# Optimization experiments

Hardware: AMD Instinct MI355X
Metric: run time of the kernel (lower is better)

## Reference

```python
import jax, jax.numpy as jnp
import numpy as np

N = 100000   # nodes
E = 1600000  # edges
F = 64       # num_features
H = 64       # hidden_units
C = 10       # num_classes
G = 1000     # graphs in batch
BN_EPS = 1e-5


def setup_inputs() -> dict:
    key = jax.random.key(0)
    ks = jax.random.split(key, 32)
    inp = {
        "x": jax.random.normal(ks[0], (N, F), dtype=jnp.float32),
        "edge_index": jax.random.randint(ks[1], (2, E), 0, N, dtype=jnp.int64),
        "batch": jnp.sort(jax.random.randint(ks[2], (N,), 0, G, dtype=jnp.int64)),
    }
    i = 3
    def w(shape, scale):
        nonlocal i
        a = jax.random.normal(ks[i], shape, dtype=jnp.float32) * scale
        i += 1
        return a
    for l, din in [(0, F), (1, H)]:
        inp[f"c{l}_w1"] = w((din, H), 1.0 / np.sqrt(din))
        inp[f"c{l}_b1"] = jnp.zeros((H,), jnp.float32)
        inp[f"c{l}_g1"] = jnp.ones((H,), jnp.float32)
        inp[f"c{l}_be1"] = jnp.zeros((H,), jnp.float32)
        inp[f"c{l}_w2"] = w((H, H), 1.0 / np.sqrt(H))
        inp[f"c{l}_b2"] = jnp.zeros((H,), jnp.float32)
        inp[f"bn{l}_g"] = jnp.ones((H,), jnp.float32)
        inp[f"bn{l}_b"] = jnp.zeros((H,), jnp.float32)
    for l, din in [(0, F), (1, H), (2, H)]:
        inp[f"l{l}_w"] = w((din, C), 1.0 / np.sqrt(din))
        inp[f"l{l}_b"] = jnp.zeros((C,), jnp.float32)
    return inp


def _bn(h, g, b):
    # BatchNorm1d in training mode: batch statistics over node axis
    m = jnp.mean(h, axis=0)
    v = jnp.var(h, axis=0)
    return g * (h - m) * jax.lax.rsqrt(v + BN_EPS) + b


def _gin_conv(h, src, dst, w1, b1, g1, be1, w2, b2):
    # scatter-add neighbor aggregation: out[dst] += h[src]; eps = 0
    agg = jax.ops.segment_sum(h[src], dst, num_segments=N)
    z = h + agg                      # (1 + eps) * x + sum_j x_j
    z = jax.nn.relu(_bn(z @ w1 + b1, g1, be1))
    return z @ w2 + b2


def reference(x, edge_index, batch,
              c0_w1, c0_b1, c0_g1, c0_be1, c0_w2, c0_b2, bn0_g, bn0_b,
              c1_w1, c1_b1, c1_g1, c1_be1, c1_w2, c1_b2, bn1_g, bn1_b,
              l0_w, l0_b, l1_w, l1_b, l2_w, l2_b):
    src, dst = edge_index[0], edge_index[1]
    h0 = x
    h1 = jax.nn.relu(_bn(_gin_conv(h0, src, dst, c0_w1, c0_b1, c0_g1, c0_be1, c0_w2, c0_b2), bn0_g, bn0_b))
    h2 = jax.nn.relu(_bn(_gin_conv(h1, src, dst, c1_w1, c1_b1, c1_g1, c1_be1, c1_w2, c1_b2), bn1_g, bn1_b))
    # jumping-knowledge readout: per-layer global_add_pool -> Linear -> sum (dropout=0)
    out = jnp.zeros((G, C), dtype=x.dtype)
    for h, w, b in [(h0, l0_w, l0_b), (h1, l1_w, l1_b), (h2, l2_w, l2_b)]:
        pooled = jax.ops.segment_sum(h, batch, num_segments=G)
        out = out + pooled @ w + b
    return out
```

## Files before the change

kernel.cpp:

```cpp
#include <hip/hip_runtime.h>
#include <hip/hip_bf16.h>

#define BN_EPS 1e-5f
#define NBMAX 512
#define CHUNK 4096
#define CAP   5120
#define PCAP  7168

typedef __hip_bfloat16 bf16;
typedef __attribute__((ext_vector_type(8))) short short8;
typedef __attribute__((ext_vector_type(4))) float f32x4;

__device__ __forceinline__ float b2f(bf16 v) { return __bfloat162float(v); }
__device__ __forceinline__ bf16 f2b(float v) { return __float2bfloat16(v); }
__device__ __forceinline__ float bl(unsigned u) { return __uint_as_float(u << 16); }
__device__ __forceinline__ float bh(unsigned u) { return __uint_as_float(u & 0xffff0000u); }
__device__ __forceinline__ unsigned pack2(float x, float y) {
    union { bf16 b[2]; unsigned u; } p;
    p.b[0] = f2b(x); p.b[1] = f2b(y);
    return p.u;
}
__device__ __forceinline__ float bs2f(short s) {
    return __uint_as_float(((unsigned)(unsigned short)s) << 16);
}
__device__ __forceinline__ short f2bs(float v) {
    bf16 b = f2b(v);
    return *reinterpret_cast<short*>(&b);
}

__global__ __launch_bounds__(256) void initcast_k(
    const float* __restrict__ in, bf16* __restrict__ out, int n4, int total4,
    int* __restrict__ bcur, int NB)
{
    if (blockIdx.x == 0) {
        for (int i = threadIdx.x; i < NB; i += 256) bcur[i] = i * CAP;
    }
    int i = blockIdx.x * 256 + threadIdx.x;
    if (i >= total4) return;
    if (i < n4) {
        float4 v = ((const float4*)in)[i];
        union { ushort4 u; bf16 b[4]; } p;
        p.b[0] = f2b(v.x); p.b[1] = f2b(v.y); p.b[2] = f2b(v.z); p.b[3] = f2b(v.w);
        ((ushort4*)out)[i] = p.u;
    } else {
        ushort4 z; z.x = 0; z.y = 0; z.z = 0; z.w = 0;
        ((ushort4*)out)[i] = z;
    }
}

__global__ __launch_bounds__(256) void binscatter_k(
    const int* __restrict__ src, const int* __restrict__ dst,
    int* __restrict__ bcur, int* __restrict__ tmp, int E, int NB)
{
    __shared__ int hist[NBMAX];
    __shared__ int loff[NBMAX];
    __shared__ int gb[NBMAX];
    __shared__ int lcur[NBMAX];
    __shared__ int staged[CHUNK];
    __shared__ unsigned short sb[CHUNK];
    __shared__ int ssc[256];
    const int t = threadIdx.x;
    for (int i = t; i < NB; i += 256) { hist[i] = 0; lcur[i] = 0; }
    __syncthreads();
    const int base = blockIdx.x * CHUNK;
    const int lim = min(CHUNK, E - base);
    int myb[16], myw[16];
    int cnt = 0;
    for (int i = t; i < lim; i += 256) {
        int d = dst[base + i];
        int s_ = src[base + i];
        int b = d >> 8;
        myb[cnt] = b;
        myw[cnt] = (s_ << 8) | (d & 255);
        cnt++;
        atomicAdd(&hist[b], 1);
    }
    __syncthreads();
    int v0 = (2 * t     < NB) ? hist[2 * t]     : 0;
    int v1 = (2 * t + 1 < NB) ? hist[2 * t + 1] : 0;
    ssc[t] = v0 + v1;
    __syncthreads();
    for (int off = 1; off < 256; off <<= 1) {
        int a = (t >= off) ? ssc[t - off] : 0;
        __syncthreads();
        ssc[t] += a;
        __syncthreads();
    }
    int excl = ssc[t] - (v0 + v1);
    if (2 * t < NB)     loff[2 * t] = excl;
    if (2 * t + 1 < NB) loff[2 * t + 1] = excl + v0;
    __syncthreads();
    for (int b = t; b < NB; b += 256)
        if (hist[b] > 0) gb[b] = atomicAdd(&bcur[b], hist[b]);
    for (int i = 0; i < cnt; i++) {
        int b = myb[i];
        int p = loff[b] + atomicAdd(&lcur[b], 1);
        staged[p] = myw[i];
        sb[p] = (unsigned short)b;
    }
    __syncthreads();
    for (int i = t; i < lim; i += 256) {
        int b = sb[i];
        tmp[gb[b] + (i - loff[b])] = staged[i];
    }
}

__global__ __launch_bounds__(256) void csr_k(
    const int* __restrict__ bcur, const int* __restrict__ tmp,
    int* __restrict__ rowptr, int* __restrict__ rowend,
    int* __restrict__ adj, int N)
{
    __shared__ int hist[256], pfx[256], cur[256], ssc[256];
    __shared__ int sadj[PCAP];
    const int b = blockIdx.x, t = threadIdx.x;
    const int lo = b * CAP;
    const int plo = b * PCAP;
    const int cnt = min(bcur[b] - lo, CAP);
    hist[t] = 0; cur[t] = 0;
    __syncthreads();
    for (int i = t; i < cnt; i += 256)
        atomicAdd(&hist[tmp[lo + i] & 255], 1);
    __syncthreads();
    const int v = hist[t];
    const int pv = (v + 7) & ~7;
    ssc[t] = pv;
    __syncthreads();
    for (int off = 1; off < 256; off <<= 1) {
        int a = (t >= off) ? ssc[t - off] : 0;
        __syncthreads();
        ssc[t] += a;
        __syncthreads();
    }
    const int myp = ssc[t] - pv;
    pfx[t] = myp;
    const int node = b * 256 + t;
    if (node < N) {
        rowptr[node] = plo + myp;
        rowend[node] = plo + myp + pv;
    }
    __syncthreads();
    const int pcnt = ssc[255];
    for (int i = t; i < cnt; i += 256) {
        int w = tmp[lo + i];
        int d = w & 255;
        int p = pfx[d] + atomicAdd(&cur[d], 1);
        sadj[p] = w >> 8;
    }
    __syncthreads();
    for (int i = v; i < pv; i++) sadj[myp + i] = N;
    __syncthreads();
    for (int i = t; i < pcnt; i += 256) adj[plo + i] = sadj[i];
}

__global__ __launch_bounds__(256, 4) void aggregate_k(
    const bf16* __restrict__ h, const int* __restrict__ rowptr,
    const int* __restrict__ rowend, const int* __restrict__ adj,
    bf16* __restrict__ z, int N)
{
    const int lane16 = threadIdx.x & 15;
    const int n = blockIdx.x * 16 + (threadIdx.x >> 4);
    if (n >= N) return;
    const char* hb_ = (const char*)h;
    const int b = rowptr[n], e = rowend[n];

    uint2 u = *(const uint2*)(hb_ + ((size_t)n << 7) + (lane16 << 3));
    float s0 = bl(u.x), s1 = bh(u.x), s2 = bl(u.y), s3 = bh(u.y);

    int m[8];
    if (b < e) {
        #pragma unroll
        for (int k = 0; k < 8; k++) m[k] = adj[b + k];
    }
    for (int i = b; i < e; ) {
        uint2 w[8];
        #pragma unroll
        for (int k = 0; k < 8; k++)
            w[k] = *(const uint2*)(hb_ + (((size_t)(unsigned)m[k]) << 7) + (lane16 << 3));
        const int inext = i + 8;
        if (inext < e) {
            #pragma unroll
            for (int k = 0; k < 8; k++) m[k] = adj[inext + k];
        }
        #pragma unroll
        for (int k = 0; k < 8; k++) {
            s0 += bl(w[k].x); s1 += bh(w[k].x);
            s2 += bl(w[k].y); s3 += bh(w[k].y);
        }
        i = inext;
    }
    uint2 o;
    o.x = pack2(s0, s1);
    o.y = pack2(s2, s3);
    *(uint2*)((char*)z + ((size_t)n << 7) + (lane16 << 3)) = o;
}

__global__ __launch_bounds__(256) void ewact_k(
    const bf16* __restrict__ y, const float* __restrict__ sc,
    const float* __restrict__ sh, bf16* __restrict__ h, int N)
{
    const int idx = blockIdx.x * 256 + threadIdx.x;
    const int total = (N + 1) * 8;
    if (idx >= total) return;
    short8 v;
    if (idx < N * 8) {
        const int f0 = (idx & 7) * 8;
        v = *(const short8*)(y + (size_t)idx * 8);
        #pragma unroll
        for (int j = 0; j < 8; j++)
            v[j] = f2bs(fmaxf(fmaf(bs2f(v[j]), sc[f0 + j], sh[f0 + j]), 0.f));
    } else {
        #pragma unroll
        for (int j = 0; j < 8; j++) v[j] = 0;
    }
    *(short8*)(h + (size_t)idx * 8) = v;
}

template<int MODE>
__global__ __launch_bounds__(256) void gemm64_k(
    const bf16* __restrict__ A,
    const float* __restrict__ scin, const float* __restrict__ shin,
    const float* __restrict__ W, const float* __restrict__ bias,
    bf16* __restrict__ out, float* __restrict__ pstat, int nrows)
{
    __shared__ bf16 sWt[64][72];
    __shared__ bf16 sC[128][68];
    __shared__ float sSc[64], sSh[64], sB[64];
    __shared__ float sredS[64][17], sredQ[64][17];
    const int tid = threadIdx.x;

    if (tid < 64) {
        sB[tid] = bias[tid];
        if (MODE == 1) { sSc[tid] = scin[tid]; sSh[tid] = shin[tid]; }
    }
    for (int i = tid; i < 4096; i += 256) {
        int k = i >> 6, n = i & 63;
        sWt[n][k] = f2b(W[i]);
    }
    __syncthreads();

    const int wave = tid >> 6, lane = tid & 63;
    const int quad = lane >> 4, l16 = lane & 15;
    const int row0 = blockIdx.x * 128 + wave * 32;

    short8 a[2][2];
    #pragma unroll
    for (int rt = 0; rt < 2; rt++) {
        int r = row0 + rt * 16 + l16;
        int rr = min(r, nrows - 1);
        const bf16* arow = A + (size_t)rr * 64;
        a[rt][0] = *(const short8*)(arow + quad * 8);
        a[rt][1] = *(const short8*)(arow + 32 + quad * 8);
        if (MODE == 1) {
            #pragma unroll
            for (int j = 0; j < 8; j++) {
                int f0 = quad * 8 + j;
                a[rt][0][j] = f2bs(fmaxf(fmaf(bs2f(a[rt][0][j]), sSc[f0], sSh[f0]), 0.f));
                int f1 = 32 + f0;
                a[rt][1][j] = f2bs(fmaxf(fmaf(bs2f(a[rt][1][j]), sSc[f1], sSh[f1]), 0.f));
            }
        }
    }

    float psS[4], psQ[4];
    #pragma unroll
    for (int t = 0; t < 4; t++) { psS[t] = 0.f; psQ[t] = 0.f; }

    #pragma unroll
    for (int t = 0; t < 4; t++) {
        const int n = t * 16 + l16;
        short8 b0 = *(const short8*)&sWt[n][quad * 8];
        short8 b1 = *(const short8*)&sWt[n][32 + quad * 8];
        const float bn_ = sB[n];
        #pragma unroll
        for (int rt = 0; rt < 2; rt++) {
            f32x4 acc = {0.f, 0.f, 0.f, 0.f};
            acc = __builtin_amdgcn_mfma_f32_16x16x32_bf16(a[rt][0], b0, acc, 0, 0, 0);
            acc = __builtin_amdgcn_mfma_f32_16x16x32_bf16(a[rt][1], b1, acc, 0, 0, 0);
            #pragma unroll
            for (int reg = 0; reg < 4; reg++) {
                const int lr = wave * 32 + rt * 16 + quad * 4 + reg;
                float v = acc[reg] + bn_;
                sC[lr][n] = f2b(v);
                if (row0 + rt * 16 + quad * 4 + reg < nrows) {
                    psS[t] += v;
                    psQ[t] = fmaf(v, v, psQ[t]);
                }
            }
        }
    }

    #pragma unroll
    for (int t = 0; t < 4; t++) {
        sredS[t * 16 + l16][wave * 4 + quad] = psS[t];
        sredQ[t * 16 + l16][wave * 4 + quad] = psQ[t];
    }
    __syncthreads();

    const int gbase = blockIdx.x * 128;
    #pragma unroll
    for (int it = 0; it < 8; it++) {
        int idx = it * 256 + tid;
        int r = idx >> 4, c4 = idx & 15;
        if (gbase + r < nrows) {
            ushort4 v = *(const ushort4*)&sC[r][c4 * 4];
            *(ushort4*)(out + (size_t)(gbase + r) * 64 + c4 * 4) = v;
        }
    }

    if (tid < 128) {
        const int c = tid & 63;
        const float* p = (tid < 64) ? &sredS[c][0] : &sredQ[c][0];
        float s = 0.f;
        #pragma unroll
        for (int i = 0; i < 16; i++) s += p[i];
        pstat[(size_t)blockIdx.x * 128 + (tid < 64 ? c : 64 + c)] = s;
    }
}

__global__ __launch_bounds__(256) void bn_reduce_k(
    const float* __restrict__ pstat, int nblk,
    const float* __restrict__ g, const float* __restrict__ be, float invN,
    float* __restrict__ sc, float* __restrict__ sh)
{
    const int f = blockIdx.x;
    const int t = threadIdx.x;
    float S = 0.f, Q = 0.f;
    for (int b = t; b < nblk; b += 256) {
        S += pstat[(size_t)b * 128 + f];
        Q += pstat[(size_t)b * 128 + 64 + f];
    }
    __shared__ float rs[256], rq[256];
    rs[t] = S; rq[t] = Q;
    __syncthreads();
    for (int off = 128; off > 0; off >>= 1) {
        if (t < off) { rs[t] += rs[t + off]; rq[t] += rq[t + off]; }
        __syncthreads();
    }
    if (t == 0) {
        float m = rs[0] * invN;
        float v = rq[0] * invN - m * m;
        float s = g[f] * rsqrtf(v + BN_EPS);
        sc[f] = s;
        sh[f] = be[f] - m * s;
    }
}

__global__ __launch_bounds__(256) void pool_readout_k(
    const bf16* __restrict__ xb, const bf16* __restrict__ h1,
    const bf16* __restrict__ y1, const int* __restrict__ batch,
    const float* __restrict__ scB, const float* __restrict__ shB,
    const float* __restrict__ w0, const float* __restrict__ b0,
    const float* __restrict__ w1, const float* __restrict__ b1,
    const float* __restrict__ w2, const float* __restrict__ b2,
    float* __restrict__ out, int Nn)
{
    const int g = blockIdx.x;
    int lo = 0, hi = Nn;
    while (lo < hi) { int mid = (lo + hi) >> 1; if (batch[mid] < g) lo = mid + 1; else hi = mid; }
    const int start = lo;
    hi = Nn;
    while (lo < hi) { int mid = (lo + hi) >> 1; if (batch[mid] <= g) lo = mid + 1; else hi = mid; }
    const int end = lo;

    const int f = threadIdx.x & 63;
    const int w = threadIdx.x >> 6;
    const float sB = scB[f], tB = shB[f];

    float s0 = 0.f, s1 = 0.f, s2 = 0.f;
    for (int i = start + w; i < end; i += 4) {
        s0 += b2f(xb[(size_t)i * 64 + f]);
        s1 += b2f(h1[(size_t)i * 64 + f]);
        s2 += fmaxf(fmaf(b2f(y1[(size_t)i * 64 + f]), sB, tB), 0.f);
    }
    __shared__ float p[3][4][64];
    p[0][w][f] = s0; p[1][w][f] = s1; p[2][w][f] = s2;
    __syncthreads();
    if (threadIdx.x < 10) {
        const int c = threadIdx.x;
        float acc = b0[c] + b1[c] + b2[c];
        for (int k = 0; k < 64; k++) {
            float q0 = p[0][0][k] + p[0][1][k] + p[0][2][k] + p[0][3][k];
            float q1 = p[1][0][k] + p[1][1][k] + p[1][2][k] + p[1][3][k];
            float q2 = p[2][0][k] + p[2][1][k] + p[2][2][k] + p[2][3][k];
            acc = fmaf(q0, w0[k * 10 + c], acc);
            acc = fmaf(q1, w1[k * 10 + c], acc);
            acc = fmaf(q2, w2[k * 10 + c], acc);
        }
        out[(size_t)g * 10 + c] = acc;
    }
}

extern "C" void kernel_launch(void* const* d_in, const int* in_sizes, int n_in,
                              void* d_out, int out_size, void* d_ws, size_t ws_size,
                              hipStream_t stream)
{
    const float* x     = (const float*)d_in[0];
    const int*   edge  = (const int*)d_in[1];
    const int*   batch = (const int*)d_in[2];
    const int N = in_sizes[0] / 64;
    const int E = in_sizes[1] / 2;
    const int G = out_size / 10;
    const int* src = edge;
    const int* dst = edge + E;
    const int NB = (N + 255) / 256;

    const float* c_w1[2]  = {(const float*)d_in[3],  (const float*)d_in[11]};
    const float* c_b1[2]  = {(const float*)d_in[4],  (const float*)d_in[12]};
    const float* c_g1[2]  = {(const float*)d_in[5],  (const float*)d_in[13]};
    const float* c_be1[2] = {(const float*)d_in[6],  (const float*)d_in[14]};
    const float* c_w2[2]  = {(const float*)d_in[7],  (const float*)d_in[15]};
    const float* c_b2[2]  = {(const float*)d_in[8],  (const float*)d_in[16]};
    const float* bn_g[2]  = {(const float*)d_in[9],  (const float*)d_in[17]};
    const float* bn_b[2]  = {(const float*)d_in[10], (const float*)d_in[18]};
    const float* lw[3]    = {(const float*)d_in[19], (const float*)d_in[21], (const float*)d_in[23]};
    const float* lb[3]    = {(const float*)d_in[20], (const float*)d_in[22], (const float*)d_in[24]};

    float* out = (float*)d_out;
    const size_t nh  = (size_t)N * 64;
    const size_t nh1 = (size_t)(N + 1) * 64;
    const int PG = (N + 127) / 128;

    bf16*  zb    = (bf16*)d_ws;
    bf16*  wb    = zb + nh;
    bf16*  xb    = wb + nh;
    bf16*  hb    = xb + nh1;
    float* scsh  = (float*)(hb + nh1);
    float* pstat = scsh + 512;
    int*   rowptr = (int*)(pstat + (size_t)PG * 128);
    int*   rowend = rowptr + N;
    int*   adj    = rowend + N;
    int*   tmp    = adj + (size_t)NB * PCAP;
    int*   bcur   = tmp + (size_t)NB * CAP;

    float* sc0 = scsh;       float* sh0 = scsh + 64;
    float* scA = scsh + 128; float* shA = scsh + 192;
    float* sc2 = scsh + 256; float* sh2 = scsh + 320;
    float* scB = scsh + 384; float* shB = scsh + 448;

    const float invN = 1.0f / (float)N;
    const int binGrid  = (E + CHUNK - 1) / CHUNK;
    const int aggGrid  = (N + 15) / 16;
    const int n4       = N * 16;
    const int total4   = (N + 1) * 16;
    const int ewGrid   = (total4 + 255) / 256;
    const int actGrid  = ((N + 1) * 8 + 255) / 256;

    initcast_k<<<ewGrid, 256, 0, stream>>>(x, xb, n4, total4, bcur, NB);
    binscatter_k<<<binGrid, 256, 0, stream>>>(src, dst, bcur, tmp, E, NB);
    csr_k<<<NB, 256, 0, stream>>>(bcur, tmp, rowptr, rowend, adj, N);

    aggregate_k<<<aggGrid, 256, 0, stream>>>(xb, rowptr, rowend, adj, zb, N);
    gemm64_k<0><<<PG, 256, 0, stream>>>(zb, nullptr, nullptr,
                                        c_w1[0], c_b1[0], zb, pstat, N);
    bn_reduce_k<<<64, 256, 0, stream>>>(pstat, PG, c_g1[0], c_be1[0], invN, sc0, sh0);
    gemm64_k<1><<<PG, 256, 0, stream>>>(zb, sc0, sh0,
                                        c_w2[0], c_b2[0], zb, pstat, N);
    bn_reduce_k<<<64, 256, 0, stream>>>(pstat, PG, bn_g[0], bn_b[0], invN, scA, shA);

    ewact_k<<<actGrid, 256, 0, stream>>>(zb, scA, shA, hb, N);

    aggregate_k<<<aggGrid, 256, 0, stream>>>(hb, rowptr, rowend, adj, wb, N);
    gemm64_k<0><<<PG, 256, 0, stream>>>(wb, nullptr, nullptr,
                                        c_w1[1], c_b1[1], wb, pstat, N);
    bn_reduce_k<<<64, 256, 0, stream>>>(pstat, PG, c_g1[1], c_be1[1], invN, sc2, sh2);
    gemm64_k<1><<<PG, 256, 0, stream>>>(wb, sc2, sh2,
                                        c_w2[1], c_b2[1], wb, pstat, N);
    bn_reduce_k<<<64, 256, 0, stream>>>(pstat, PG, bn_g[1], bn_b[1], invN, scB, shB);

    pool_readout_k<<<G, 256, 0, stream>>>(xb, hb, wb, batch,
                                          scB, shB,
                                          lw[0], lb[0], lw[1], lb[1], lw[2], lb[2],
                                          out, N);
}
```

Before: 292.4 us.

## Fuse GIN MLP, BatchNorm reductions and activation into cooperative grid-synced kernel

Replaces the per-layer sequence of two GEMM kernels, two BN-reduce kernels and the elementwise activation kernel with one cooperative kernel. It uses grid.sync to compute BatchNorm statistics in place, and it recomputes the first GEMM so the intermediate never goes to global memory. This removes several launches and one full read/write of the hidden tensor per layer. The cost is computing the first GEMM twice, a serial per-block reduction over 256 partials, and two grid-wide barriers. The pooling readout is also revectorized, using 16 row groups with 8-byte loads.

```diff
diff --git a/kernel.cpp b/kernel.cpp
--- a/kernel.cpp
+++ b/kernel.cpp
@@ -1,5 +1,8 @@
 #include <hip/hip_runtime.h>
 #include <hip/hip_bf16.h>
+#include <hip/hip_cooperative_groups.h>
+
+namespace cg = cooperative_groups;
 
 #define BN_EPS 1e-5f
 #define NBMAX 512
@@ -29,11 +32,15 @@
 }
 
 __global__ __launch_bounds__(256) void initcast_k(
-    const float* __restrict__ in, bf16* __restrict__ out, int n4, int total4,
-    int* __restrict__ bcur, int NB)
+    const float* __restrict__ in, bf16* __restrict__ xb, bf16* __restrict__ hb,
+    int n4, int total4, int* __restrict__ bcur, int NB)
 {
     if (blockIdx.x == 0) {
         for (int i = threadIdx.x; i < NB; i += 256) bcur[i] = i * CAP;
+        if (threadIdx.x < 16) {
+            ushort4 z; z.x = 0; z.y = 0; z.z = 0; z.w = 0;
+            ((ushort4*)hb)[(size_t)n4 + threadIdx.x] = z;
+        }
     }
     int i = blockIdx.x * 256 + threadIdx.x;
     if (i >= total4) return;
@@ -41,10 +48,10 @@
         float4 v = ((const float4*)in)[i];
         union { ushort4 u; bf16 b[4]; } p;
         p.b[0] = f2b(v.x); p.b[1] = f2b(v.y); p.b[2] = f2b(v.z); p.b[3] = f2b(v.w);
-        ((ushort4*)out)[i] = p.u;
+        ((ushort4*)xb)[i] = p.u;
     } else {
         ushort4 z; z.x = 0; z.y = 0; z.z = 0; z.w = 0;
-        ((ushort4*)out)[i] = z;
+        ((ushort4*)xb)[i] = z;
     }
 }
 
@@ -194,154 +201,230 @@
     *(uint2*)((char*)z + ((size_t)n << 7) + (lane16 << 3)) = o;
 }
 
-__global__ __launch_bounds__(256) void ewact_k(
-    const bf16* __restrict__ y, const float* __restrict__ sc,
-    const float* __restrict__ sh, bf16* __restrict__ h, int N)
-{
-    const int idx = blockIdx.x * 256 + threadIdx.x;
-    const int total = (N + 1) * 8;
-    if (idx >= total) return;
-    short8 v;
-    if (idx < N * 8) {
-        const int f0 = (idx & 7) * 8;
-        v = *(const short8*)(y + (size_t)idx * 8);
-        #pragma unroll
-        for (int j = 0; j < 8; j++)
-            v[j] = f2bs(fmaxf(fmaf(bs2f(v[j]), sc[f0 + j], sh[f0 + j]), 0.f));
-    } else {
-        #pragma unroll
-        for (int j = 0; j < 8; j++) v[j] = 0;
-    }
-    *(short8*)(h + (size_t)idx * 8) = v;
-}
-
-template<int MODE>
-__global__ __launch_bounds__(256) void gemm64_k(
-    const bf16* __restrict__ A,
-    const float* __restrict__ scin, const float* __restrict__ shin,
-    const float* __restrict__ W, const float* __restrict__ bias,
-    bf16* __restrict__ out, float* __restrict__ pstat, int nrows)
-{
-    __shared__ bf16 sWt[64][72];
-    __shared__ bf16 sC[128][68];
-    __shared__ float sSc[64], sSh[64], sB[64];
+template<int L>
+__global__ __launch_bounds__(256) void mlp_k(
+    const bf16* __restrict__ A, bf16* __restrict__ Y, bf16* __restrict__ H,
+    const float* __restrict__ W1, const float* __restrict__ B1,
+    const float* __restrict__ G1, const float* __restrict__ BE1,
+    const float* __restrict__ W2, const float* __restrict__ B2,
+    const float* __restrict__ G2, const float* __restrict__ BE2,
+    float* __restrict__ pstat, float* __restrict__ pstat2,
+    float* __restrict__ scB, float* __restrict__ shB,
+    int N, int RPB, float invN, int GRID)
+{
+    cg::grid_group grid = cg::this_grid();
+    __shared__ bf16 sWt1[64][72], sWt2[64][72];
+    __shared__ bf16 sT[128][68];
     __shared__ float sredS[64][17], sredQ[64][17];
+    __shared__ float sSc[64], sSh[64], sB1[64], sB2[64];
     const int tid = threadIdx.x;
 
-    if (tid < 64) {
-        sB[tid] = bias[tid];
-        if (MODE == 1) { sSc[tid] = scin[tid]; sSh[tid] = shin[tid]; }
-    }
+    if (tid < 64) { sB1[tid] = B1[tid]; sB2[tid] = B2[tid]; }
     for (int i = tid; i < 4096; i += 256) {
         int k = i >> 6, n = i & 63;
-        sWt[n][k] = f2b(W[i]);
-    }
-    __syncthreads();
-
+        sWt1[n][k] = f2b(W1[i]);
+        sWt2[n][k] = f2b(W2[i]);
+    }
+    __syncthreads();
+
+    const int blk = blockIdx.x;
+    const int r0 = blk * RPB;
+    const int rEnd = min(N, r0 + RPB);
+    const int CH = (RPB + 127) >> 7;
     const int wave = tid >> 6, lane = tid & 63;
     const int quad = lane >> 4, l16 = lane & 15;
-    const int row0 = blockIdx.x * 128 + wave * 32;
-
-    short8 a[2][2];
-    #pragma unroll
-    for (int rt = 0; rt < 2; rt++) {
-        int r = row0 + rt * 16 + l16;
-        int rr = min(r, nrows - 1);
-        const bf16* arow = A + (size_t)rr * 64;
-        a[rt][0] = *(const short8*)(arow + quad * 8);
-        a[rt][1] = *(const short8*)(arow + 32 + quad * 8);
-        if (MODE == 1) {
-            #pragma unroll
-            for (int j = 0; j < 8; j++) {
-                int f0 = quad * 8 + j;
-                a[rt][0][j] = f2bs(fmaxf(fmaf(bs2f(a[rt][0][j]), sSc[f0], sSh[f0]), 0.f));
-                int f1 = 32 + f0;
-                a[rt][1][j] = f2bs(fmaxf(fmaf(bs2f(a[rt][1][j]), sSc[f1], sSh[f1]), 0.f));
-            }
-        }
-    }
 
     float psS[4], psQ[4];
     #pragma unroll
     for (int t = 0; t < 4; t++) { psS[t] = 0.f; psQ[t] = 0.f; }
 
-    #pragma unroll
-    for (int t = 0; t < 4; t++) {
-        const int n = t * 16 + l16;
-        short8 b0 = *(const short8*)&sWt[n][quad * 8];
-        short8 b1 = *(const short8*)&sWt[n][32 + quad * 8];
-        const float bn_ = sB[n];
+    for (int c = 0; c < CH; c++) {
+        const int rbase = r0 + c * 128 + wave * 32;
+        short8 a[2][2];
         #pragma unroll
         for (int rt = 0; rt < 2; rt++) {
-            f32x4 acc = {0.f, 0.f, 0.f, 0.f};
-            acc = __builtin_amdgcn_mfma_f32_16x16x32_bf16(a[rt][0], b0, acc, 0, 0, 0);
-            acc = __builtin_amdgcn_mfma_f32_16x16x32_bf16(a[rt][1], b1, acc, 0, 0, 0);
+            int r = rbase + rt * 16 + l16;
+            int rr = min(r, rEnd - 1);
+            const bf16* arow = A + (size_t)rr * 64;
+            a[rt][0] = *(const short8*)(arow + quad * 8);
+            a[rt][1] = *(const short8*)(arow + 32 + quad * 8);
+        }
+        #pragma unroll
+        for (int t = 0; t < 4; t++) {
+            const int n = t * 16 + l16;
+            short8 b0 = *(const short8*)&sWt1[n][quad * 8];
+            short8 b1 = *(const short8*)&sWt1[n][32 + quad * 8];
+            const float bn_ = sB1[n];
             #pragma unroll
-            for (int reg = 0; reg < 4; reg++) {
-                const int lr = wave * 32 + rt * 16 + quad * 4 + reg;
-                float v = acc[reg] + bn_;
-                sC[lr][n] = f2b(v);
-                if (row0 + rt * 16 + quad * 4 + reg < nrows) {
-                    psS[t] += v;
-                    psQ[t] = fmaf(v, v, psQ[t]);
+            for (int rt = 0; rt < 2; rt++) {
+                f32x4 acc = {0.f, 0.f, 0.f, 0.f};
+                acc = __builtin_amdgcn_mfma_f32_16x16x32_bf16(a[rt][0], b0, acc, 0, 0, 0);
+                acc = __builtin_amdgcn_mfma_f32_16x16x32_bf16(a[rt][1], b1, acc, 0, 0, 0);
+                #pragma unroll
+                for (int reg = 0; reg < 4; reg++) {
+                    const int grow = rbase + rt * 16 + quad * 4 + reg;
+                    float v = acc[reg] + bn_;
+                    if (grow < rEnd) { psS[t] += v; psQ[t] = fmaf(v, v, psQ[t]); }
                 }
             }
         }
     }
-
     #pragma unroll
     for (int t = 0; t < 4; t++) {
         sredS[t * 16 + l16][wave * 4 + quad] = psS[t];
         sredQ[t * 16 + l16][wave * 4 + quad] = psQ[t];
     }
     __syncthreads();
-
-    const int gbase = blockIdx.x * 128;
-    #pragma unroll
-    for (int it = 0; it < 8; it++) {
-        int idx = it * 256 + tid;
-        int r = idx >> 4, c4 = idx & 15;
-        if (gbase + r < nrows) {
-            ushort4 v = *(const ushort4*)&sC[r][c4 * 4];
-            *(ushort4*)(out + (size_t)(gbase + r) * 64 + c4 * 4) = v;
-        }
-    }
-
     if (tid < 128) {
         const int c = tid & 63;
         const float* p = (tid < 64) ? &sredS[c][0] : &sredQ[c][0];
         float s = 0.f;
         #pragma unroll
         for (int i = 0; i < 16; i++) s += p[i];
-        pstat[(size_t)blockIdx.x * 128 + (tid < 64 ? c : 64 + c)] = s;
-    }
-}
-
-__global__ __launch_bounds__(256) void bn_reduce_k(
-    const float* __restrict__ pstat, int nblk,
-    const float* __restrict__ g, const float* __restrict__ be, float invN,
-    float* __restrict__ sc, float* __restrict__ sh)
-{
-    const int f = blockIdx.x;
-    const int t = threadIdx.x;
-    float S = 0.f, Q = 0.f;
-    for (int b = t; b < nblk; b += 256) {
-        S += pstat[(size_t)b * 128 + f];
-        Q += pstat[(size_t)b * 128 + 64 + f];
-    }
-    __shared__ float rs[256], rq[256];
-    rs[t] = S; rq[t] = Q;
-    __syncthreads();
-    for (int off = 128; off > 0; off >>= 1) {
-        if (t < off) { rs[t] += rs[t + off]; rq[t] += rq[t + off]; }
-        __syncthreads();
-    }
-    if (t == 0) {
-        float m = rs[0] * invN;
-        float v = rq[0] * invN - m * m;
-        float s = g[f] * rsqrtf(v + BN_EPS);
-        sc[f] = s;
-        sh[f] = be[f] - m * s;
+        pstat[(size_t)blk * 128 + (tid < 64 ? c : 64 + c)] = s;
+    }
+    grid.sync();
+
+    if (tid < 64) {
+        float S = 0.f, Q = 0.f;
+        for (int b = 0; b < GRID; b++) {
+            S += pstat[(size_t)b * 128 + tid];
+            Q += pstat[(size_t)b * 128 + 64 + tid];
+        }
+        float m = S * invN;
+        float var = Q * invN - m * m;
+        float s = G1[tid] * rsqrtf(var + BN_EPS);
+        sSc[tid] = s;
+        sSh[tid] = BE1[tid] - m * s;
+    }
+    __syncthreads();
+
+    #pragma unroll
+    for (int t = 0; t < 4; t++) { psS[t] = 0.f; psQ[t] = 0.f; }
+
+    for (int c = 0; c < CH; c++) {
+        const int rbase = r0 + c * 128 + wave * 32;
+        short8 a[2][2];
+        #pragma unroll
+        for (int rt = 0; rt < 2; rt++) {
+            int r = rbase + rt * 16 + l16;
+            int rr = min(r, rEnd - 1);
+            const bf16* arow = A + (size_t)rr * 64;
+            a[rt][0] = *(const short8*)(arow + quad * 8);
+            a[rt][1] = *(const short8*)(arow + 32 + quad * 8);
+        }
+        #pragma unroll
+        for (int t = 0; t < 4; t++) {
+            const int n = t * 16 + l16;
+            short8 b0 = *(const short8*)&sWt1[n][quad * 8];
+            short8 b1 = *(const short8*)&sWt1[n][32 + quad * 8];
+            const float bn_ = sB1[n];
+            const float sc = sSc[n], sh = sSh[n];
+            #pragma unroll
+            for (int rt = 0; rt < 2; rt++) {
+                f32x4 acc = {0.f, 0.f, 0.f, 0.f};
+                acc = __builtin_amdgcn_mfma_f32_16x16x32_bf16(a[rt][0], b0, acc, 0, 0, 0);
+                acc = __builtin_amdgcn_mfma_f32_16x16x32_bf16(a[rt][1], b1, acc, 0, 0, 0);
+                #pragma unroll
+                for (int reg = 0; reg < 4; reg++) {
+                    const int lr = wave * 32 + rt * 16 + quad * 4 + reg;
+                    float v = acc[reg] + bn_;
+                    sT[lr][n] = f2b(fmaxf(fmaf(v, sc, sh), 0.f));
+                }
+            }
+        }
+        short8 a2[2][2];
+        #pragma unroll
+        for (int rt = 0; rt < 2; rt++) {
+            const int lr = wave * 32 + rt * 16 + l16;
+            a2[rt][0] = *(const short8*)&sT[lr][quad * 8];
+            a2[rt][1] = *(const short8*)&sT[lr][32 + quad * 8];
+        }
+        #pragma unroll
+        for (int t = 0; t < 4; t++) {
+            const int n = t * 16 + l16;
+            short8 b0 = *(const short8*)&sWt2[n][quad * 8];
+            short8 b1 = *(const short8*)&sWt2[n][32 + quad * 8];
+            const float bn_ = sB2[n];
+            #pragma unroll
+            for (int rt = 0; rt < 2; rt++) {
+                f32x4 acc = {0.f, 0.f, 0.f, 0.f};
+                acc = __builtin_amdgcn_mfma_f32_16x16x32_bf16(a2[rt][0], b0, acc, 0, 0, 0);
+                acc = __builtin_amdgcn_mfma_f32_16x16x32_bf16(a2[rt][1], b1, acc, 0, 0, 0);
+                #pragma unroll
+                for (int reg = 0; reg < 4; reg++) {
+                    const int lr = wave * 32 + rt * 16 + quad * 4 + reg;
+                    const int grow = rbase + rt * 16 + quad * 4 + reg;
+                    float v = acc[reg] + bn_;
+                    sT[lr][n] = f2b(v);
+                    if (grow < rEnd) { psS[t] += v; psQ[t] = fmaf(v, v, psQ[t]); }
+                }
+            }
+        }
+        __syncthreads();
+        const int gbase = r0 + c * 128;
+        #pragma unroll
+        for (int it = 0; it < 8; it++) {
+            int idx = it * 256 + tid;
+            int r = idx >> 4, c4 = idx & 15;
+            if (gbase + r < rEnd) {
+                ushort4 v = *(const ushort4*)&sT[r][c4 * 4];
+                *(ushort4*)(Y + (size_t)(gbase + r) * 64 + c4 * 4) = v;
+            }
+        }
+        __syncthreads();
+    }
+    #pragma unroll
+    for (int t = 0; t < 4; t++) {
+        sredS[t * 16 + l16][wave * 4 + quad] = psS[t];
+        sredQ[t * 16 + l16][wave * 4 + quad] = psQ[t];
+    }
+    __syncthreads();
+    if (tid < 128) {
+        const int c = tid & 63;
+        const float* p = (tid < 64) ? &sredS[c][0] : &sredQ[c][0];
+        float s = 0.f;
+        #pragma unroll
+        for (int i = 0; i < 16; i++) s += p[i];
+        pstat2[(size_t)blk * 128 + (tid < 64 ? c : 64 + c)] = s;
+    }
+    grid.sync();
+
+    if (L == 0) {
+        if (tid < 64) {
+            float S = 0.f, Q = 0.f;
+            for (int b = 0; b < GRID; b++) {
+                S += pstat2[(size_t)b * 128 + tid];
+                Q += pstat2[(size_t)b * 128 + 64 + tid];
+            }
+            float m = S * invN;
+            float var = Q * invN - m * m;
+            float s = G2[tid] * rsqrtf(var + BN_EPS);
+            sSc[tid] = s;
+            sSh[tid] = BE2[tid] - m * s;
+        }
+        __syncthreads();
+        for (int idx = r0 * 8 + tid; idx < rEnd * 8; idx += 256) {
+            const int f0 = (idx & 7) * 8;
+            short8 v = *(const short8*)(Y + (size_t)idx * 8);
+            #pragma unroll
+            for (int j = 0; j < 8; j++)
+                v[j] = f2bs(fmaxf(fmaf(bs2f(v[j]), sSc[f0 + j], sSh[f0 + j]), 0.f));
+            *(short8*)(H + (size_t)idx * 8) = v;
+        }
+    } else {
+        if (blk == 0 && tid < 64) {
+            float S = 0.f, Q = 0.f;
+            for (int b = 0; b < GRID; b++) {
+                S += pstat2[(size_t)b * 128 + tid];
+                Q += pstat2[(size_t)b * 128 + 64 + tid];
+            }
+            float m = S * invN;
+            float var = Q * invN - m * m;
+            float s = G2[tid] * rsqrtf(var + BN_EPS);
+            scB[tid] = s;
+            shB[tid] = BE2[tid] - m * s;
+        }
     }
 }
 
@@ -354,6 +437,13 @@
     const float* __restrict__ w2, const float* __restrict__ b2,
     float* __restrict__ out, int Nn)
 {
+    __shared__ float sB2[2][64];
+    __shared__ float p[3][16][64];
+    __shared__ float q[3][64];
+    const int tid = threadIdx.x;
+    if (tid < 64) { sB2[0][tid] = scB[tid]; sB2[1][tid] = shB[tid]; }
+    __syncthreads();
+
     const int g = blockIdx.x;
     int lo = 0, hi = Nn;
     while (lo < hi) { int mid = (lo + hi) >> 1; if (batch[mid] < g) lo = mid + 1; else hi = mid; }
@@ -362,29 +452,49 @@
     while (lo < hi) { int mid = (lo + hi) >> 1; if (batch[mid] <= g) lo = mid + 1; else hi = mid; }
     const int end = lo;
 
-    const int f = threadIdx.x & 63;
-    const int w = threadIdx.x >> 6;
-    const float sB = scB[f], tB = shB[f];
-
-    float s0 = 0.f, s1 = 0.f, s2 = 0.f;
-    for (int i = start + w; i < end; i += 4) {
-        s0 += b2f(xb[(size_t)i * 64 + f]);
-        s1 += b2f(h1[(size_t)i * 64 + f]);
-        s2 += fmaxf(fmaf(b2f(y1[(size_t)i * 64 + f]), sB, tB), 0.f);
-    }
-    __shared__ float p[3][4][64];
-    p[0][w][f] = s0; p[1][w][f] = s1; p[2][w][f] = s2;
-    __syncthreads();
-    if (threadIdx.x < 10) {
-        const int c = threadIdx.x;
+    const int l16 = tid & 15, grp = tid >> 4;
+    const int f0 = l16 * 4;
+    const float scB0 = sB2[0][f0],      shB0 = sB2[1][f0];
+    const float scB1 = sB2[0][f0 + 1],  shB1 = sB2[1][f0 + 1];
+    const float scB2_ = sB2[0][f0 + 2], shB2_ = sB2[1][f0 + 2];
+    const float scB3 = sB2[0][f0 + 3],  shB3 = sB2[1][f0 + 3];
+
+    float a0 = 0.f, a1 = 0.f, a2 = 0.f, a3 = 0.f;
+    float h0 = 0.f, h1s = 0.f, h2 = 0.f, h3 = 0.f;
+    float c0 = 0.f, c1 = 0.f, c2 = 0.f, c3 = 0.f;
+    for (int i = start + grp; i < end; i += 16) {
+        const size_t ro = (size_t)i * 16 + l16;
+        uint2 ux = ((const uint2*)xb)[ro];
+        uint2 u0 = ((const uint2*)h1)[ro];
+        uint2 u1 = ((const uint2*)y1)[ro];
+        a0 += bl(ux.x); a1 += bh(ux.x); a2 += bl(ux.y); a3 += bh(ux.y);
+        h0 += bl(u0.x); h1s += bh(u0.x); h2 += bl(u0.y); h3 += bh(u0.y);
+        c0 += fmaxf(fmaf(bl(u1.x), scB0, shB0), 0.f);
+        c1 += fmaxf(fmaf(bh(u1.x), scB1, shB1), 0.f);
+        c2 += fmaxf(fmaf(bl(u1.y), scB2_, shB2_), 0.f);
+        c3 += fmaxf(fmaf(bh(u1.y), scB3, shB3), 0.f);
+    }
+    p[0][grp][f0] = a0; p[0][grp][f0 + 1] = a1; p[0][grp][f0 + 2] = a2; p[0][grp][f0 + 3] = a3;
+    p[1][grp][f0] = h0; p[1][grp][f0 + 1] = h1s; p[1][grp][f0 + 2] = h2; p[1][grp][f0 + 3] = h3;
+    p[2][grp][f0] = c0; p[2][grp][f0 + 1] = c1; p[2][grp][f0 + 2] = c2; p[2][grp][f0 + 3] = c3;
+    __syncthreads();
+
+    if (tid < 192) {
+        const int arr = tid >> 6, f = tid & 63;
+        float s = 0.f;
+        #pragma unroll
+        for (int i = 0; i < 16; i++) s += p[arr][i][f];
+        q[arr][f] = s;
+    }
+    __syncthreads();
+
+    if (tid < 10) {
+        const int c = tid;
         float acc = b0[c] + b1[c] + b2[c];
         for (int k = 0; k < 64; k++) {
-            float q0 = p[0][0][k] + p[0][1][k] + p[0][2][k] + p[0][3][k];
-            float q1 = p[1][0][k] + p[1][1][k] + p[1][2][k] + p[1][3][k];
-            float q2 = p[2][0][k] + p[2][1][k] + p[2][2][k] + p[2][3][k];
-            acc = fmaf(q0, w0[k * 10 + c], acc);
-            acc = fmaf(q1, w1[k * 10 + c], acc);
-            acc = fmaf(q2, w2[k * 10 + c], acc);
+            acc = fmaf(q[0][k], w0[k * 10 + c], acc);
+            acc = fmaf(q[1][k], w1[k * 10 + c], acc);
+            acc = fmaf(q[2][k], w2[k * 10 + c], acc);
         }
         out[(size_t)g * 10 + c] = acc;
     }
@@ -416,56 +526,65 @@
     const float* lb[3]    = {(const float*)d_in[20], (const float*)d_in[22], (const float*)d_in[24]};
 
     float* out = (float*)d_out;
-    const size_t nh  = (size_t)N * 64;
     const size_t nh1 = (size_t)(N + 1) * 64;
-    const int PG = (N + 127) / 128;
+    const int GRID_MLP = 256;
+    const int RPB = (N + GRID_MLP - 1) / GRID_MLP;
 
     bf16*  zb    = (bf16*)d_ws;
-    bf16*  wb    = zb + nh;
-    bf16*  xb    = wb + nh;
+    bf16*  wb    = zb + nh1;
+    bf16*  xb    = wb + nh1;
     bf16*  hb    = xb + nh1;
     float* scsh  = (float*)(hb + nh1);
-    float* pstat = scsh + 512;
-    int*   rowptr = (int*)(pstat + (size_t)PG * 128);
+    float* pstat  = scsh + 512;
+    float* pstat2 = pstat + (size_t)GRID_MLP * 128;
+    int*   rowptr = (int*)(pstat2 + (size_t)GRID_MLP * 128);
     int*   rowend = rowptr + N;
     int*   adj    = rowend + N;
     int*   tmp    = adj + (size_t)NB * PCAP;
     int*   bcur   = tmp + (size_t)NB * CAP;
 
-    float* sc0 = scsh;       float* sh0 = scsh + 64;
-    float* scA = scsh + 128; float* shA = scsh + 192;
-    float* sc2 = scsh + 256; float* sh2 = scsh + 320;
     float* scB = scsh + 384; float* shB = scsh + 448;
 
-    const float invN = 1.0f / (float)N;
+    float invN = 1.0f / (float)N;
     const int binGrid  = (E + CHUNK - 1) / CHUNK;
     const int aggGrid  = (N + 15) / 16;
     const int n4       = N * 16;
     const int total4   = (N + 1) * 16;
     const int ewGrid   = (total4 + 255) / 256;
-    const int actGrid  = ((N + 1) * 8 + 255) / 256;
-
-    initcast_k<<<ewGrid, 256, 0, stream>>>(x, xb, n4, total4, bcur, NB);
+
+    initcast_k<<<ewGrid, 256, 0, stream>>>(x, xb, hb, n4, total4, bcur, NB);
     binscatter_k<<<binGrid, 256, 0, stream>>>(src, dst, bcur, tmp, E, NB);
     csr_k<<<NB, 256, 0, stream>>>(bcur, tmp, rowptr, rowend, adj, N);
 
     aggregate_k<<<aggGrid, 256, 0, stream>>>(xb, rowptr, rowend, adj, zb, N);
-    gemm64_k<0><<<PG, 256, 0, stream>>>(zb, nullptr, nullptr,
-                                        c_w1[0], c_b1[0], zb, pstat, N);
-    bn_reduce_k<<<64, 256, 0, stream>>>(pstat, PG, c_g1[0], c_be1[0], invN, sc0, sh0);
-    gemm64_k<1><<<PG, 256, 0, stream>>>(zb, sc0, sh0,
-                                        c_w2[0], c_b2[0], zb, pstat, N);
-    bn_reduce_k<<<64, 256, 0, stream>>>(pstat, PG, bn_g[0], bn_b[0], invN, scA, shA);
-
-    ewact_k<<<actGrid, 256, 0, stream>>>(zb, scA, shA, hb, N);
+    {
+        const bf16* A = zb; bf16* Y = zb; bf16* H = hb;
+        const float *W1 = c_w1[0], *B1 = c_b1[0], *G1 = c_g1[0], *BE1 = c_be1[0];
+        const float *W2 = c_w2[0], *B2 = c_b2[0], *G2 = bn_g[0], *BE2 = bn_b[0];
+        int Nv = N, RPBv = RPB, GRIDv = GRID_MLP;
+        void* args[] = {(void*)&A, (void*)&Y, (void*)&H,
+                        (void*)&W1, (void*)&B1, (void*)&G1, (void*)&BE1,
+                        (void*)&W2, (void*)&B2, (void*)&G2, (void*)&BE2,
+                        (void*)&pstat, (void*)&pstat2, (void*)&scB, (void*)&shB,
+                        (void*)&Nv, (void*)&RPBv, (void*)&invN, (void*)&GRIDv};
+        hipLaunchCooperativeKernel((const void*)mlp_k<0>, dim3(GRID_MLP), dim3(256),
+                                   args, 0, stream);
+    }
 
     aggregate_k<<<aggGrid, 256, 0, stream>>>(hb, rowptr, rowend, adj, wb, N);
-    gemm64_k<0><<<PG, 256, 0, stream>>>(wb, nullptr, nullptr,
-                                        c_w1[1], c_b1[1], wb, pstat, N);
-    bn_reduce_k<<<64, 256, 0, stream>>>(pstat, PG, c_g1[1], c_be1[1], invN, sc2, sh2);
-    gemm64_k<1><<<PG, 256, 0, stream>>>(wb, sc2, sh2,
-                                        c_w2[1], c_b2[1], wb, pstat, N);
-    bn_reduce_k<<<64, 256, 0, stream>>>(pstat, PG, bn_g[1], bn_b[1], invN, scB, shB);
+    {
+        const bf16* A = wb; bf16* Y = wb; bf16* H = hb;
+        const float *W1 = c_w1[1], *B1 = c_b1[1], *G1 = c_g1[1], *BE1 = c_be1[1];
+        const float *W2 = c_w2[1], *B2 = c_b2[1], *G2 = bn_g[1], *BE2 = bn_b[1];
+        int Nv = N, RPBv = RPB, GRIDv = GRID_MLP;
+        void* args[] = {(void*)&A, (void*)&Y, (void*)&H,
+                        (void*)&W1, (void*)&B1, (void*)&G1, (void*)&BE1,
+                        (void*)&W2, (void*)&B2, (void*)&G2, (void*)&BE2,
+                        (void*)&pstat, (void*)&pstat2, (void*)&scB, (void*)&shB,
+                        (void*)&Nv, (void*)&RPBv, (void*)&invN, (void*)&GRIDv};
+        hipLaunchCooperativeKernel((const void*)mlp_k<1>, dim3(GRID_MLP), dim3(256),
+                                   args, 0, stream);
+    }
 
     pool_readout_k<<<G, 256, 0, stream>>>(xb, hb, wb, batch,
                                           scB, shB,
```

New measurement: 676.7 us. 2.31x slower.

## Fuse BN stat reduction into GEMM via last-block atomic; vectorize pooling

Applied to the files above, without the earlier changes.

Removes the four separate bn_reduce kernel launches. Each GEMM block now bumps an atomic counter, and the last block to finish reduces all per-block partial stats into the BN scale and shift. The pooling readout kernel now reads 4 bf16 features per thread with 16 row groups instead of scalar loads over 4 groups, which raises memory-level parallelism. The trade-off is a serial tail where one block reduces roughly 782 partials, and the counters must be zeroed in initcast every call.

```diff
diff --git a/kernel.cpp b/kernel.cpp
--- a/kernel.cpp
+++ b/kernel.cpp
@@ -30,10 +30,11 @@
 
 __global__ __launch_bounds__(256) void initcast_k(
     const float* __restrict__ in, bf16* __restrict__ out, int n4, int total4,
-    int* __restrict__ bcur, int NB)
+    int* __restrict__ bcur, int NB, int* __restrict__ cnts)
 {
     if (blockIdx.x == 0) {
         for (int i = threadIdx.x; i < NB; i += 256) bcur[i] = i * CAP;
+        if (threadIdx.x < 4) cnts[threadIdx.x] = 0;
     }
     int i = blockIdx.x * 256 + threadIdx.x;
     if (i >= total4) return;
@@ -220,12 +221,17 @@
     const bf16* __restrict__ A,
     const float* __restrict__ scin, const float* __restrict__ shin,
     const float* __restrict__ W, const float* __restrict__ bias,
-    bf16* __restrict__ out, float* __restrict__ pstat, int nrows)
+    bf16* __restrict__ out, float* __restrict__ pstat, int nrows,
+    const float* __restrict__ gr, const float* __restrict__ be, float invN,
+    float* __restrict__ scout, float* __restrict__ shout,
+    int* __restrict__ counter, int nblk)
 {
     __shared__ bf16 sWt[64][72];
     __shared__ bf16 sC[128][68];
     __shared__ float sSc[64], sSh[64], sB[64];
     __shared__ float sredS[64][17], sredQ[64][17];
+    __shared__ float red2[2][128];
+    __shared__ int isLast;
     const int tid = threadIdx.x;
 
     if (tid < 64) {
@@ -315,33 +321,34 @@
         for (int i = 0; i < 16; i++) s += p[i];
         pstat[(size_t)blockIdx.x * 128 + (tid < 64 ? c : 64 + c)] = s;
     }
-}
-
-__global__ __launch_bounds__(256) void bn_reduce_k(
-    const float* __restrict__ pstat, int nblk,
-    const float* __restrict__ g, const float* __restrict__ be, float invN,
-    float* __restrict__ sc, float* __restrict__ sh)
-{
-    const int f = blockIdx.x;
-    const int t = threadIdx.x;
-    float S = 0.f, Q = 0.f;
-    for (int b = t; b < nblk; b += 256) {
-        S += pstat[(size_t)b * 128 + f];
-        Q += pstat[(size_t)b * 128 + 64 + f];
-    }
-    __shared__ float rs[256], rq[256];
-    rs[t] = S; rq[t] = Q;
-    __syncthreads();
-    for (int off = 128; off > 0; off >>= 1) {
-        if (t < off) { rs[t] += rs[t + off]; rq[t] += rq[t + off]; }
-        __syncthreads();
-    }
-    if (t == 0) {
-        float m = rs[0] * invN;
-        float v = rq[0] * invN - m * m;
-        float s = g[f] * rsqrtf(v + BN_EPS);
-        sc[f] = s;
-        sh[f] = be[f] - m * s;
+
+    __threadfence();
+    __syncthreads();
+    if (tid == 0) isLast = (atomicAdd(counter, 1) == nblk - 1);
+    __syncthreads();
+    if (!isLast) return;
+    __threadfence();
+    const int c = tid & 127, part = tid >> 7;
+    float s = 0.f;
+    int b = part;
+    for (; b + 8 <= nblk; b += 8) {
+        float x0 = pstat[(size_t)(b)     * 128 + c];
+        float x1 = pstat[(size_t)(b + 2) * 128 + c];
+        float x2 = pstat[(size_t)(b + 4) * 128 + c];
+        float x3 = pstat[(size_t)(b + 6) * 128 + c];
+        s += (x0 + x1) + (x2 + x3);
+    }
+    for (; b < nblk; b += 2) s += pstat[(size_t)b * 128 + c];
+    red2[part][c] = s;
+    __syncthreads();
+    if (tid < 64) {
+        float S = red2[0][tid] + red2[1][tid];
+        float Q = red2[0][64 + tid] + red2[1][64 + tid];
+        float m = S * invN;
+        float var = Q * invN - m * m;
+        float sc_ = gr[tid] * rsqrtf(var + BN_EPS);
+        scout[tid] = sc_;
+        shout[tid] = be[tid] - m * sc_;
     }
 }
 
@@ -354,6 +361,13 @@
     const float* __restrict__ w2, const float* __restrict__ b2,
     float* __restrict__ out, int Nn)
 {
+    __shared__ float sB2[2][64];
+    __shared__ float p[3][16][64];
+    __shared__ float q[3][64];
+    const int tid = threadIdx.x;
+    if (tid < 64) { sB2[0][tid] = scB[tid]; sB2[1][tid] = shB[tid]; }
+    __syncthreads();
+
     const int g = blockIdx.x;
     int lo = 0, hi = Nn;
     while (lo < hi) { int mid = (lo + hi) >> 1; if (batch[mid] < g) lo = mid + 1; else hi = mid; }
@@ -362,29 +376,49 @@
     while (lo < hi) { int mid = (lo + hi) >> 1; if (batch[mid] <= g) lo = mid + 1; else hi = mid; }
     const int end = lo;
 
-    const int f = threadIdx.x & 63;
-    const int w = threadIdx.x >> 6;
-    const float sB = scB[f], tB = shB[f];
-
-    float s0 = 0.f, s1 = 0.f, s2 = 0.f;
-    for (int i = start + w; i < end; i += 4) {
-        s0 += b2f(xb[(size_t)i * 64 + f]);
-        s1 += b2f(h1[(size_t)i * 64 + f]);
-        s2 += fmaxf(fmaf(b2f(y1[(size_t)i * 64 + f]), sB, tB), 0.f);
-    }
-    __shared__ float p[3][4][64];
-    p[0][w][f] = s0; p[1][w][f] = s1; p[2][w][f] = s2;
-    __syncthreads();
-    if (threadIdx.x < 10) {
-        const int c = threadIdx.x;
+    const int l16 = tid & 15, grp = tid >> 4;
+    const int f0 = l16 * 4;
+    const float scB0 = sB2[0][f0],      shB0 = sB2[1][f0];
+    const float scB1 = sB2[0][f0 + 1],  shB1 = sB2[1][f0 + 1];
+    const float scB2_ = sB2[0][f0 + 2], shB2_ = sB2[1][f0 + 2];
+    const float scB3 = sB2[0][f0 + 3],  shB3 = sB2[1][f0 + 3];
+
+    float a0 = 0.f, a1 = 0.f, a2 = 0.f, a3 = 0.f;
+    float h0 = 0.f, h1s = 0.f, h2 = 0.f, h3 = 0.f;
+    float c0 = 0.f, c1 = 0.f, c2 = 0.f, c3 = 0.f;
+    for (int i = start + grp; i < end; i += 16) {
+        const size_t ro = (size_t)i * 16 + l16;
+        uint2 ux = ((const uint2*)xb)[ro];
+        uint2 u0 = ((const uint2*)h1)[ro];
+        uint2 u1 = ((const uint2*)y1)[ro];
+        a0 += bl(ux.x); a1 += bh(ux.x); a2 += bl(ux.y); a3 += bh(ux.y);
+        h0 += bl(u0.x); h1s += bh(u0.x); h2 += bl(u0.y); h3 += bh(u0.y);
+        c0 += fmaxf(fmaf(bl(u1.x), scB0, shB0), 0.f);
+        c1 += fmaxf(fmaf(bh(u1.x), scB1, shB1), 0.f);
+        c2 += fmaxf(fmaf(bl(u1.y), scB2_, shB2_), 0.f);
+        c3 += fmaxf(fmaf(bh(u1.y), scB3, shB3), 0.f);
+    }
+    p[0][grp][f0] = a0; p[0][grp][f0 + 1] = a1; p[0][grp][f0 + 2] = a2; p[0][grp][f0 + 3] = a3;
+    p[1][grp][f0] = h0; p[1][grp][f0 + 1] = h1s; p[1][grp][f0 + 2] = h2; p[1][grp][f0 + 3] = h3;
+    p[2][grp][f0] = c0; p[2][grp][f0 + 1] = c1; p[2][grp][f0 + 2] = c2; p[2][grp][f0 + 3] = c3;
+    __syncthreads();
+
+    if (tid < 192) {
+        const int arr = tid >> 6, f = tid & 63;
+        float s = 0.f;
+        #pragma unroll
+        for (int i = 0; i < 16; i++) s += p[arr][i][f];
+        q[arr][f] = s;
+    }
+    __syncthreads();
+
+    if (tid < 10) {
+        const int c = tid;
         float acc = b0[c] + b1[c] + b2[c];
         for (int k = 0; k < 64; k++) {
-            float q0 = p[0][0][k] + p[0][1][k] + p[0][2][k] + p[0][3][k];
-            float q1 = p[1][0][k] + p[1][1][k] + p[1][2][k] + p[1][3][k];
-            float q2 = p[2][0][k] + p[2][1][k] + p[2][2][k] + p[2][3][k];
-            acc = fmaf(q0, w0[k * 10 + c], acc);
-            acc = fmaf(q1, w1[k * 10 + c], acc);
-            acc = fmaf(q2, w2[k * 10 + c], acc);
+            acc = fmaf(q[0][k], w0[k * 10 + c], acc);
+            acc = fmaf(q[1][k], w1[k * 10 + c], acc);
+            acc = fmaf(q[2][k], w2[k * 10 + c], acc);
         }
         out[(size_t)g * 10 + c] = acc;
     }
@@ -416,13 +450,12 @@
     const float* lb[3]    = {(const float*)d_in[20], (const float*)d_in[22], (const float*)d_in[24]};
 
     float* out = (float*)d_out;
-    const size_t nh  = (size_t)N * 64;
     const size_t nh1 = (size_t)(N + 1) * 64;
     const int PG = (N + 127) / 128;
 
     bf16*  zb    = (bf16*)d_ws;
-    bf16*  wb    = zb + nh;
-    bf16*  xb    = wb + nh;
+    bf16*  wb    = zb + nh1;
+    bf16*  xb    = wb + nh1;
     bf16*  hb    = xb + nh1;
     float* scsh  = (float*)(hb + nh1);
     float* pstat = scsh + 512;
@@ -431,6 +464,7 @@
     int*   adj    = rowend + N;
     int*   tmp    = adj + (size_t)NB * PCAP;
     int*   bcur   = tmp + (size_t)NB * CAP;
+    int*   cnts   = bcur + NB;
 
     float* sc0 = scsh;       float* sh0 = scsh + 64;
     float* scA = scsh + 128; float* shA = scsh + 192;
@@ -445,27 +479,27 @@
     const int ewGrid   = (total4 + 255) / 256;
     const int actGrid  = ((N + 1) * 8 + 255) / 256;
 
-    initcast_k<<<ewGrid, 256, 0, stream>>>(x, xb, n4, total4, bcur, NB);
+    initcast_k<<<ewGrid, 256, 0, stream>>>(x, xb, n4, total4, bcur, NB, cnts);
     binscatter_k<<<binGrid, 256, 0, stream>>>(src, dst, bcur, tmp, E, NB);
     csr_k<<<NB, 256, 0, stream>>>(bcur, tmp, rowptr, rowend, adj, N);
 
     aggregate_k<<<aggGrid, 256, 0, stream>>>(xb, rowptr, rowend, adj, zb, N);
     gemm64_k<0><<<PG, 256, 0, stream>>>(zb, nullptr, nullptr,
-                                        c_w1[0], c_b1[0], zb, pstat, N);
-    bn_reduce_k<<<64, 256, 0, stream>>>(pstat, PG, c_g1[0], c_be1[0], invN, sc0, sh0);
+                                        c_w1[0], c_b1[0], zb, pstat, N,
+                                        c_g1[0], c_be1[0], invN, sc0, sh0, cnts + 0, PG);
     gemm64_k<1><<<PG, 256, 0, stream>>>(zb, sc0, sh0,
-                                        c_w2[0], c_b2[0], zb, pstat, N);
-    bn_reduce_k<<<64, 256, 0, stream>>>(pstat, PG, bn_g[0], bn_b[0], invN, scA, shA);
+                                        c_w2[0], c_b2[0], zb, pstat, N,
+                                        bn_g[0], bn_b[0], invN, scA, shA, cnts + 1, PG);
 
     ewact_k<<<actGrid, 256, 0, stream>>>(zb, scA, shA, hb, N);
 
     aggregate_k<<<aggGrid, 256, 0, stream>>>(hb, rowptr, rowend, adj, wb, N);
     gemm64_k<0><<<PG, 256, 0, stream>>>(wb, nullptr, nullptr,
-                                        c_w1[1], c_b1[1], wb, pstat, N);
-    bn_reduce_k<<<64, 256, 0, stream>>>(pstat, PG, c_g1[1], c_be1[1], invN, sc2, sh2);
+                                        c_w1[1], c_b1[1], wb, pstat, N,
+                                        c_g1[1], c_be1[1], invN, sc2, sh2, cnts + 2, PG);
     gemm64_k<1><<<PG, 256, 0, stream>>>(wb, sc2, sh2,
-                                        c_w2[1], c_b2[1], wb, pstat, N);
-    bn_reduce_k<<<64, 256, 0, stream>>>(pstat, PG, bn_g[1], bn_b[1], invN, scB, shB);
+                                        c_w2[1], c_b2[1], wb, pstat, N,
+                                        bn_g[1], bn_b[1], invN, scB, shB, cnts + 3, PG);
 
     pool_readout_k<<<G, 256, 0, stream>>>(xb, hb, wb, batch,
                                           scB, shB,
```

Result: slower. 675.7 us (+131.1%).
